# Performance work log

Hardware: AMD Instinct MI355X
Metric: run time of the kernel (lower is better)

Reference implementation:

```python
import jax, jax.numpy as jnp
import numpy as np
from jax import lax

N_TRIALS = 4096
N_T = 2000
DT = 0.001
LEAK_RATE = 0.01      # leak=True
TIME_CONSTANT = 0.01  # time_dependence=True
VARIANCE = 1.0


def setup_inputs() -> dict:
    key = jax.random.key(0)
    k1, k2 = jax.random.split(key)
    stimulus = jax.random.normal(k1, (N_TRIALS, N_T), dtype=jnp.float32)
    noise = jax.random.normal(k2, (N_TRIALS, N_T), dtype=jnp.float32)
    return {
        "stimulus": stimulus,
        "noise": noise,
        "a": jnp.float32(2.0),
        "z": jnp.float32(0.5),
        "drift_gain": jnp.float32(7.0),
        "drift_offset": jnp.float32(0.0),
        "beta": jnp.float32(50.0),
    }


def reference(stimulus, noise, a, z, drift_gain, drift_offset, beta):
    n_trials, n_t = stimulus.shape
    starting_point = z * a
    drift_rates = drift_gain * stimulus + drift_offset
    scaled_noise = noise * jnp.sqrt(jnp.float32(VARIANCE * DT))
    # evidence[t] = decay * evidence[t-1] + u[t-1]
    # where decay = 1 - leak_rate*dt (constant) and
    # u[i] = drift[i]*dt + noise[i] + leak_rate*starting_point*dt
    decay = jnp.float32(1.0 - LEAK_RATE * DT)
    u = drift_rates * DT + scaled_noise + LEAK_RATE * starting_point * DT  # (n_trials, n_t)

    def step(e_prev, u_t):
        e_new = decay * e_prev + u_t
        return e_new, e_new

    e0 = starting_point * jnp.ones((n_trials,), dtype=stimulus.dtype)
    # steps t=1..n_t-1 consume u[:, t-1]
    _, ev_rest = lax.scan(step, e0, jnp.swapaxes(u[:, : n_t - 1], 0, 1))  # (n_t-1, n_trials)
    evidence = jnp.concatenate([e0[None, :], ev_rest], axis=0).T  # (n_trials, n_t)

    urgency = jnp.arange(n_t, dtype=stimulus.dtype) * TIME_CONSTANT  # (n_t,)
    dv = urgency[None, :] * (evidence - starting_point) + starting_point
    h1 = jax.nn.sigmoid(beta * (dv - a))
    h0 = jax.nn.sigmoid(-beta * dv)
    return dv, h1, h0
```

## Files before the change

### kernel.cpp

```cpp
#include <hip/hip_runtime.h>
#include <math.h>

#define N_T   2000
#define NG    500
#define WAVES 4

typedef float vf4 __attribute__((ext_vector_type(4)));

__global__ __launch_bounds__(256, 4) void ddm_kernel(
    const float* __restrict__ stim,
    const float* __restrict__ noise,
    const float* __restrict__ a_p,
    const float* __restrict__ z_p,
    const float* __restrict__ gain_p,
    const float* __restrict__ off_p,
    const float* __restrict__ beta_p,
    float* __restrict__ out,
    int n_trials)
{
    const int wave  = threadIdx.x >> 6;
    const int lane  = threadIdx.x & 63;
    const int trial = blockIdx.x * WAVES + wave;
    if (trial >= n_trials) return;

    constexpr float DT   = 0.001f;
    constexpr float LEAK = 0.01f;
    constexpr float DEC  = 1.0f - LEAK * DT;
    constexpr float INV  = 1.0f / DEC;
    constexpr float De2 = DEC * DEC, De3 = De2 * DEC, De4 = De2 * De2;
    constexpr float I2  = INV * INV, I3  = I2 * INV, I4  = I2 * I2;
    constexpr float D8 = De4 * De4, D16 = D8 * D8, D32 = D16 * D16,
                    D64 = D32 * D32, D128 = D64 * D64, D256 = D128 * D128;
    constexpr float I8 = I4 * I4, I16 = I8 * I8, I32 = I16 * I16,
                    I64 = I32 * I32, I128 = I64 * I64, I256 = I128 * I128;

    const float a    = *a_p;
    const float z    = *z_p;
    const float gain = *gain_p;
    const float offs = *off_p;
    const float beta = *beta_p;

    const float sp = z * a;
    const float C1 = gain * DT;
    const float C2 = sqrtf(1.0f * DT);
    const float C3 = offs * DT + LEAK * sp * DT;

    float dl = 1.f, il = 1.f, bd = De4, bi = I4;
    int nb = lane;
#pragma unroll
    for (int b = 0; b < 6; ++b) {
        if (nb & 1) { dl *= bd; il *= bi; }
        bd *= bd; bi *= bi; nb >>= 1;
    }
    il *= INV;

    const float* srow = stim  + (size_t)trial * N_T;
    const float* nrow = noise + (size_t)trial * N_T;

    vf4 sv[8], nv[8];
#pragma unroll
    for (int j = 0; j < 8; ++j) {
        const int g  = j * 64 + lane;
        const int gc = (g < NG) ? g : (NG - 1);
        sv[j] = __builtin_nontemporal_load((const vf4*)(srow + 4 * gc));
        nv[j] = __builtin_nontemporal_load((const vf4*)(nrow + 4 * gc));
    }

    float l0[8], l1[8], l2[8], l3[8];
    {
        float ifj = il;
#pragma unroll
        for (int j = 0; j < 8; ++j) {
            const float m = ((j * 64 + lane) < NG) ? 1.f : 0.f;
            const float u0 = C1 * sv[j].x + C2 * nv[j].x + C3;
            const float u1 = C1 * sv[j].y + C2 * nv[j].y + C3;
            const float u2 = C1 * sv[j].z + C2 * nv[j].z + C3;
            const float u3 = C1 * sv[j].w + C2 * nv[j].w + C3;
            const float w0 = u0 * ifj * m;
            const float w1 = u1 * (ifj * INV) * m;
            const float w2 = u2 * (ifj * I2) * m;
            const float w3 = u3 * (ifj * I3) * m;
            l0[j] = w0;
            l1[j] = l0[j] + w1;
            l2[j] = l1[j] + w2;
            l3[j] = l2[j] + w3;
            ifj *= I256;
        }
    }

    float sc[8];
#pragma unroll
    for (int j = 0; j < 8; ++j) sc[j] = l3[j];
#pragma unroll
    for (int off = 1; off < 64; off <<= 1) {
        float v[8];
#pragma unroll
        for (int j = 0; j < 8; ++j) v[j] = __shfl_up(sc[j], off, 64);
#pragma unroll
        for (int j = 0; j < 8; ++j) sc[j] += (lane >= off) ? v[j] : 0.f;
    }

    float S0[8];
    {
        float c = 0.f;
#pragma unroll
        for (int j = 0; j < 8; ++j) {
            const float btot = __shfl(sc[j], 63, 64);
            S0[j] = c + (sc[j] - l3[j]);
            c += btot;
        }
    }

    float* dv_out = out;
    float* h1_out = out + (size_t)n_trials * N_T;
    float* h0_out = out + 2 * (size_t)n_trials * N_T;
    const size_t rbase = (size_t)trial * N_T;

    float dpj = dl;
#pragma unroll
    for (int j = 0; j < 8; ++j) {
        const int  g     = j * 64 + lane;
        const bool valid = g < NG;
        const int  t0    = 4 * g;

        const float e0 = dpj *         (sp + S0[j]);
        const float e1 = (dpj * DEC) * (sp + S0[j] + l0[j]);
        const float e2 = (dpj * De2) * (sp + S0[j] + l1[j]);
        const float e3 = (dpj * De3) * (sp + S0[j] + l2[j]);

        vf4 dv4, h14, h04;
        dv4.x = (float)(t0    ) * 0.01f * (e0 - sp) + sp;
        dv4.y = (float)(t0 + 1) * 0.01f * (e1 - sp) + sp;
        dv4.z = (float)(t0 + 2) * 0.01f * (e2 - sp) + sp;
        dv4.w = (float)(t0 + 3) * 0.01f * (e3 - sp) + sp;
#pragma unroll
        for (int q = 0; q < 4; ++q) {
            const float dv = dv4[q];
            h14[q] = __builtin_amdgcn_rcpf(1.0f + __expf(-beta * (dv - a)));
            h04[q] = __builtin_amdgcn_rcpf(1.0f + __expf( beta * dv));
        }

        if (valid) {
            const size_t base = rbase + (size_t)t0;
            __builtin_nontemporal_store(dv4, (vf4*)(dv_out + base));
            __builtin_nontemporal_store(h14, (vf4*)(h1_out + base));
            __builtin_nontemporal_store(h04, (vf4*)(h0_out + base));
        }
        dpj *= D256;
    }
}

extern "C" void kernel_launch(void* const* d_in, const int* in_sizes, int n_in,
                              void* d_out, int out_size, void* d_ws, size_t ws_size,
                              hipStream_t stream) {
    const float* stim  = (const float*)d_in[0];
    const float* noise = (const float*)d_in[1];
    const float* a_p   = (const float*)d_in[2];
    const float* z_p   = (const float*)d_in[3];
    const float* g_p   = (const float*)d_in[4];
    const float* o_p   = (const float*)d_in[5];
    const float* b_p   = (const float*)d_in[6];
    float* outp = (float*)d_out;

    const int n_trials = in_sizes[0] / N_T;
    const int blocks = (n_trials + WAVES - 1) / WAVES;
    ddm_kernel<<<blocks, 256, 0, stream>>>(stim, noise, a_p, z_p, g_p, o_p, b_p,
                                           outp, n_trials);
}
```

Before: 158.1 us.

## Split each trial's scan across two waves with shared-memory carry

Each trial is now handled by two wavefronts, each covering half of the 2000 time steps, instead of one wave per trial. The first half's total is passed through shared memory after a block barrier, and the second half adds it as a carry-in using precomputed decay powers. This halves per-thread register arrays so the launch bound can allow more occupancy, and doubles the number of blocks. The cost is a __syncthreads, an LDS exchange, and slightly more numerical drift from the carry composition.

Result: no change. 158.0 us (-0.1%).

```diff
diff --git a/kernel.cpp b/kernel.cpp
--- a/kernel.cpp
+++ b/kernel.cpp
@@ -1,13 +1,13 @@
 #include <hip/hip_runtime.h>
 #include <math.h>
 
-#define N_T   2000
-#define NG    500
-#define WAVES 4
+#define N_T 2000
+#define NG  500
+#define TRIALS_PER_BLOCK 2
 
 typedef float vf4 __attribute__((ext_vector_type(4)));
 
-__global__ __launch_bounds__(256, 4) void ddm_kernel(
+__global__ __launch_bounds__(256, 5) void ddm_kernel(
     const float* __restrict__ stim,
     const float* __restrict__ noise,
     const float* __restrict__ a_p,
@@ -18,10 +18,14 @@
     float* __restrict__ out,
     int n_trials)
 {
-    const int wave  = threadIdx.x >> 6;
-    const int lane  = threadIdx.x & 63;
-    const int trial = blockIdx.x * WAVES + wave;
-    if (trial >= n_trials) return;
+    __shared__ float half_tot[TRIALS_PER_BLOCK];
+
+    const int wid  = threadIdx.x >> 6;
+    const int lane = threadIdx.x & 63;
+    const int tloc = wid >> 1;
+    const int half = wid & 1;
+    int trial = blockIdx.x * TRIALS_PER_BLOCK + tloc;
+    if (trial >= n_trials) trial = n_trials - 1;
 
     constexpr float DT   = 0.001f;
     constexpr float LEAK = 0.01f;
@@ -33,6 +37,8 @@
                     D64 = D32 * D32, D128 = D64 * D64, D256 = D128 * D128;
     constexpr float I8 = I4 * I4, I16 = I8 * I8, I32 = I16 * I16,
                     I64 = I32 * I32, I128 = I64 * I64, I256 = I128 * I128;
+    constexpr float D1024 = D256 * D256 * D256 * D256;
+    constexpr float I1024 = I256 * I256 * I256 * I256;
 
     const float a    = *a_p;
     const float z    = *z_p;
@@ -53,25 +59,28 @@
         bd *= bd; bi *= bi; nb >>= 1;
     }
     il *= INV;
+    const float dlh = half ? dl * D1024 : dl;
+    const float ilh = half ? il * I1024 : il;
 
     const float* srow = stim  + (size_t)trial * N_T;
     const float* nrow = noise + (size_t)trial * N_T;
+    const int gbase = half * 256;
 
-    vf4 sv[8], nv[8];
+    vf4 sv[4], nv[4];
 #pragma unroll
-    for (int j = 0; j < 8; ++j) {
-        const int g  = j * 64 + lane;
+    for (int j = 0; j < 4; ++j) {
+        const int g  = gbase + j * 64 + lane;
         const int gc = (g < NG) ? g : (NG - 1);
         sv[j] = __builtin_nontemporal_load((const vf4*)(srow + 4 * gc));
         nv[j] = __builtin_nontemporal_load((const vf4*)(nrow + 4 * gc));
     }
 
-    float l0[8], l1[8], l2[8], l3[8];
+    float l0[4], l1[4], l2[4], l3[4];
     {
-        float ifj = il;
+        float ifj = ilh;
 #pragma unroll
-        for (int j = 0; j < 8; ++j) {
-            const float m = ((j * 64 + lane) < NG) ? 1.f : 0.f;
+        for (int j = 0; j < 4; ++j) {
+            const float m = ((gbase + j * 64 + lane) < NG) ? 1.f : 0.f;
             const float u0 = C1 * sv[j].x + C2 * nv[j].x + C3;
             const float u1 = C1 * sv[j].y + C2 * nv[j].y + C3;
             const float u2 = C1 * sv[j].z + C2 * nv[j].z + C3;
@@ -88,51 +97,55 @@
         }
     }
 
-    float sc[8];
+    float sc[4];
 #pragma unroll
-    for (int j = 0; j < 8; ++j) sc[j] = l3[j];
+    for (int j = 0; j < 4; ++j) sc[j] = l3[j];
 #pragma unroll
     for (int off = 1; off < 64; off <<= 1) {
-        float v[8];
+        float v[4];
 #pragma unroll
-        for (int j = 0; j < 8; ++j) v[j] = __shfl_up(sc[j], off, 64);
+        for (int j = 0; j < 4; ++j) v[j] = __shfl_up(sc[j], off, 64);
 #pragma unroll
-        for (int j = 0; j < 8; ++j) sc[j] += (lane >= off) ? v[j] : 0.f;
+        for (int j = 0; j < 4; ++j) sc[j] += (lane >= off) ? v[j] : 0.f;
     }
 
-    float S0[8];
-    {
-        float c = 0.f;
+    float S0[4];
+    float c = 0.f;
 #pragma unroll
-        for (int j = 0; j < 8; ++j) {
-            const float btot = __shfl(sc[j], 63, 64);
-            S0[j] = c + (sc[j] - l3[j]);
-            c += btot;
-        }
+    for (int j = 0; j < 4; ++j) {
+        const float btot = __shfl(sc[j], 63, 64);
+        S0[j] = c + (sc[j] - l3[j]);
+        c += btot;
     }
+
+    if (!half && lane == 0) half_tot[tloc] = c;
+    __syncthreads();
+    const float cin = half ? half_tot[tloc] : 0.f;
 
     float* dv_out = out;
     float* h1_out = out + (size_t)n_trials * N_T;
     float* h0_out = out + 2 * (size_t)n_trials * N_T;
     const size_t rbase = (size_t)trial * N_T;
+    const float spc = sp;
 
-    float dpj = dl;
+    float dpj = dlh;
 #pragma unroll
-    for (int j = 0; j < 8; ++j) {
-        const int  g     = j * 64 + lane;
+    for (int j = 0; j < 4; ++j) {
+        const int  g     = gbase + j * 64 + lane;
         const bool valid = g < NG;
         const int  t0    = 4 * g;
+        const float Sb   = spc + cin + S0[j];
 
-        const float e0 = dpj *         (sp + S0[j]);
-        const float e1 = (dpj * DEC) * (sp + S0[j] + l0[j]);
-        const float e2 = (dpj * De2) * (sp + S0[j] + l1[j]);
-        const float e3 = (dpj * De3) * (sp + S0[j] + l2[j]);
+        const float e0 = dpj *         (Sb);
+        const float e1 = (dpj * DEC) * (Sb + l0[j]);
+        const float e2 = (dpj * De2) * (Sb + l1[j]);
+        const float e3 = (dpj * De3) * (Sb + l2[j]);
 
         vf4 dv4, h14, h04;
-        dv4.x = (float)(t0    ) * 0.01f * (e0 - sp) + sp;
-        dv4.y = (float)(t0 + 1) * 0.01f * (e1 - sp) + sp;
-        dv4.z = (float)(t0 + 2) * 0.01f * (e2 - sp) + sp;
-        dv4.w = (float)(t0 + 3) * 0.01f * (e3 - sp) + sp;
+        dv4.x = (float)(t0    ) * 0.01f * (e0 - spc) + spc;
+        dv4.y = (float)(t0 + 1) * 0.01f * (e1 - spc) + spc;
+        dv4.z = (float)(t0 + 2) * 0.01f * (e2 - spc) + spc;
+        dv4.w = (float)(t0 + 3) * 0.01f * (e3 - spc) + spc;
 #pragma unroll
         for (int q = 0; q < 4; ++q) {
             const float dv = dv4[q];
@@ -163,7 +176,7 @@
     float* outp = (float*)d_out;
 
     const int n_trials = in_sizes[0] / N_T;
-    const int blocks = (n_trials + WAVES - 1) / WAVES;
+    const int blocks = (n_trials + TRIALS_PER_BLOCK - 1) / TRIALS_PER_BLOCK;
     ddm_kernel<<<blocks, 256, 0, stream>>>(stim, noise, a_p, z_p, g_p, o_p, b_p,
                                            outp, n_trials);
 }
```
